# Optimization experiments

Hardware: AMD Instinct MI355X
Metric: run time of the kernel (lower is better)

## Reference

```python
import jax, jax.numpy as jnp
import numpy as np

B, D, H, L, P, IMG = 8, 768, 12, 12, 16, 448
GRID = 28  # pos_embed grid (785 = 1 + 28*28)
EPS = 1e-5


def layer_norm(x, g, b):
    mu = jnp.mean(x, axis=-1, keepdims=True)
    var = jnp.mean((x - mu) ** 2, axis=-1, keepdims=True)
    return (x - mu) * jax.lax.rsqrt(var + EPS) * g + b


def setup_inputs() -> dict:
    key = jax.random.key(0)
    ks = jax.random.split(key, 12)
    s = 0.02
    inp = {
        "x": jax.random.normal(ks[0], (B, 3, IMG, IMG), dtype=jnp.float32),
        "conv_w": jax.random.normal(ks[1], (D, 3, P, P), dtype=jnp.float32) * s,
        "conv_b": jnp.zeros((D,), jnp.float32),
        "cls_token": jax.random.normal(ks[2], (1, 1, D), dtype=jnp.float32) * s,
        "pos_embed": jax.random.normal(ks[3], (1, 1 + GRID * GRID, D), dtype=jnp.float32) * s,
        "ln1_g": jnp.ones((L, D), jnp.float32),
        "ln1_b": jnp.zeros((L, D), jnp.float32),
        "qkv_w": jax.random.normal(ks[4], (L, D, 3 * D), dtype=jnp.float32) * s,
        "qkv_b": jnp.zeros((L, 3 * D), jnp.float32),
        "proj_w": jax.random.normal(ks[5], (L, D, D), dtype=jnp.float32) * s,
        "proj_b": jnp.zeros((L, D), jnp.float32),
        "ln2_g": jnp.ones((L, D), jnp.float32),
        "ln2_b": jnp.zeros((L, D), jnp.float32),
        "mlp_w1": jax.random.normal(ks[6], (L, D, 4 * D), dtype=jnp.float32) * s,
        "mlp_b1": jnp.zeros((L, 4 * D), jnp.float32),
        "mlp_w2": jax.random.normal(ks[7], (L, 4 * D, D), dtype=jnp.float32) * s,
        "mlp_b2": jnp.zeros((L, D), jnp.float32),
        "lnf_g": jnp.ones((D,), jnp.float32),
        "lnf_b": jnp.zeros((D,), jnp.float32),
    }
    return inp


def _vit_forward(x, conv_w, conv_b, cls_token, pos_embed,
                 ln1_g, ln1_b, qkv_w, qkv_b, proj_w, proj_b,
                 ln2_g, ln2_b, mlp_w1, mlp_b1, mlp_w2, mlp_b2, lnf_g, lnf_b):
    b = x.shape[0]
    # PatchEmbed: strided conv -> [B, D, 28, 28] -> [B, N, D]
    h = jax.lax.conv_general_dilated(
        x, conv_w, window_strides=(P, P), padding="VALID",
        dimension_numbers=("NCHW", "OIHW", "NCHW")) + conv_b[None, :, None, None]
    gh, gw = h.shape[2], h.shape[3]
    h = h.reshape(b, D, gh * gw).transpose(0, 2, 1)  # [B, N, D]
    # ClassEmbed
    h = jnp.concatenate([jnp.broadcast_to(cls_token, (b, 1, D)), h], axis=1)
    # PosEmbed with bicubic interpolation of the grid part (identity when gh=gw=28)
    grid = pos_embed[:, 1:, :].transpose(0, 2, 1).reshape(1, D, GRID, GRID)
    grid = jax.image.resize(grid, (1, D, gh, gw), method="bicubic")
    grid = grid.reshape(1, D, gh * gw).transpose(0, 2, 1)
    pos = jnp.concatenate([pos_embed[:, :1, :], grid], axis=1)
    h = h + pos

    scale = (D // H) ** (-0.5)

    def block(h, p):
        (l1g, l1b, qw, qb, pw, pb, l2g, l2b, w1, b1, w2, b2) = p
        y = layer_norm(h, l1g, l1b)
        m, n, d = y.shape
        qkv = (y @ qw + qb).reshape(m, n, 3, H, d // H)
        qkv = qkv.transpose(2, 0, 3, 1, 4)  # [3, B, H, N, dh]
        q, k, v = qkv[0], qkv[1], qkv[2]
        w = jax.nn.softmax(jnp.einsum("bhnd,bhmd->bhnm", q, k) * scale, axis=-1)
        attn = jnp.einsum("bhnm,bhmd->bhnd", w, v).transpose(0, 2, 1, 3).reshape(m, n, d)
        h = h + (attn @ pw + pb)
        y = layer_norm(h, l2g, l2b)
        h = h + (jax.nn.gelu(y @ w1 + b1, approximate=False) @ w2 + b2)
        return h, None

    params = (ln1_g, ln1_b, qkv_w, qkv_b, proj_w, proj_b,
              ln2_g, ln2_b, mlp_w1, mlp_b1, mlp_w2, mlp_b2)
    h, _ = jax.lax.scan(block, h, params)
    return layer_norm(h, lnf_g, lnf_b)[:, 0]


def reference(x, conv_w, conv_b, cls_token, pos_embed,
              ln1_g, ln1_b, qkv_w, qkv_b, proj_w, proj_b,
              ln2_g, ln2_b, mlp_w1, mlp_b1, mlp_w2, mlp_b2, lnf_g, lnf_b):
    return _vit_forward(x, conv_w, conv_b, cls_token, pos_embed,
                        ln1_g, ln1_b, qkv_w, qkv_b, proj_w, proj_b,
                        ln2_g, ln2_b, mlp_w1, mlp_b1, mlp_w2, mlp_b2, lnf_g, lnf_b)
```

## Files before the change

kernel.cpp:

```cpp
#include <hip/hip_runtime.h>
#include <math.h>

#define B_   8
#define D_   768
#define H_   12
#define L_   12
#define NTOK 785
#define NPAT 784
#define MTOT (B_ * NTOK)
#define MPAT (B_ * NPAT)
#define MPAD 6400
#define DFF  3072
#define EPS_ 1e-5f

typedef unsigned short u16;
typedef unsigned int   u32;
typedef short s16x8 __attribute__((ext_vector_type(8)));
typedef float f32x4 __attribute__((ext_vector_type(4)));

__device__ __forceinline__ u16 f2b(float f) {
    u32 u = __float_as_uint(f);
    u += 0x7fffu + ((u >> 16) & 1u);
    return (u16)(u >> 16);
}
__device__ __forceinline__ float b2f(u16 s) {
    return __uint_as_float(((u32)s) << 16);
}
__device__ __forceinline__ void gload_lds16(const void* g, void* l) {
    __builtin_amdgcn_global_load_lds(
        (const __attribute__((address_space(1))) void*)g,
        (__attribute__((address_space(3))) void*)l, 16, 0, 0);
}
__device__ __forceinline__ float gelu_exact(float x) {
    return 0.5f * x * (1.0f + erff(x * 0.70710678118654752f));
}

template <int BM, int MODE, int OUTBF>
__global__ __launch_bounds__(256) void mfma_gemm(
    const u16* __restrict__ A, const u16* __restrict__ WT,
    const float* __restrict__ bias, const float* __restrict__ R,
    void* __restrict__ Cout, int M, int N, int K)
{
    constexpr int MI = BM / 32;
    __shared__ u16 As[2][BM * 32];
    __shared__ u16 Bs[2][128 * 32];

    const int bm = blockIdx.y * BM;
    const int bn = blockIdx.x * 128;
    const int t  = threadIdx.x;
    const int wv = t >> 6, ln = t & 63;
    const int wr = wv >> 1, wc = wv & 1;

    f32x4 acc[MI][4];
    const f32x4 z4 = {0.f, 0.f, 0.f, 0.f};
#pragma unroll
    for (int i = 0; i < MI; i++)
#pragma unroll
        for (int j = 0; j < 4; j++) acc[i][j] = z4;

    const int lrow = ln & 15;
    const int sq   = ((ln >> 4) ^ (ln & 3)) * 8;
    const int ssl  = ((ln & 3) ^ ((ln >> 2) & 3)) * 8;

    auto stage = [&](int kt, int buf) {
#pragma unroll
        for (int g = 0; g < BM / 64; g++) {
            const int c = g * 256 + wv * 64 + ln;
            const int r = c >> 2;
            u16* ldsA = As[buf] + (g * 256 + wv * 64) * 8;
            gload_lds16(A + (size_t)(bm + r) * K + kt + ssl, ldsA);
        }
#pragma unroll
        for (int g = 0; g < 2; g++) {
            const int c = g * 256 + wv * 64 + ln;
            const int r = c >> 2;
            u16* ldsB = Bs[buf] + (g * 256 + wv * 64) * 8;
            gload_lds16(WT + (size_t)(bn + r) * K + kt + ssl, ldsB);
        }
    };

    stage(0, 0);
    __syncthreads();
    int cur = 0;

    for (int kt = 0; kt < K; kt += 32) {
        if (kt + 32 < K) stage(kt + 32, cur ^ 1);

        s16x8 af[MI], bf[4];
#pragma unroll
        for (int i = 0; i < MI; i++)
            af[i] = *(const s16x8*)(As[cur] + (wr * (BM / 2) + i * 16 + lrow) * 32 + sq);
#pragma unroll
        for (int j = 0; j < 4; j++)
            bf[j] = *(const s16x8*)(Bs[cur] + (wc * 64 + j * 16 + lrow) * 32 + sq);
#pragma unroll
        for (int i = 0; i < MI; i++)
#pragma unroll
            for (int j = 0; j < 4; j++)
                acc[i][j] = __builtin_amdgcn_mfma_f32_16x16x32_bf16(
                    af[i], bf[j], acc[i][j], 0, 0, 0);

        __syncthreads();
        cur ^= 1;
    }

    const int col_l = ln & 15;
    const int rq    = (ln >> 4) * 4;
#pragma unroll
    for (int j = 0; j < 4; j++) {
        const int col = bn + wc * 64 + j * 16 + col_l;
        const float bj = bias[col];
#pragma unroll
        for (int i = 0; i < MI; i++) {
            const int row0 = bm + wr * (BM / 2) + i * 16 + rq;
#pragma unroll
            for (int rg = 0; rg < 4; rg++) {
                const int row = row0 + rg;
                if (row >= M) continue;
                float v = acc[i][j][rg] + bj;
                if (MODE == 1) v = gelu_exact(v);
                if (MODE == 2) v += R[(size_t)row * N + col];
                if (OUTBF) ((u16*)Cout)[(size_t)row * N + col] = f2b(v);
                else       ((float*)Cout)[(size_t)row * N + col] = v;
            }
        }
    }
}

__global__ __launch_bounds__(256) void wt_kernel(
    const float* __restrict__ W, u16* __restrict__ WT, int K, int N)
{
    const size_t lz = blockIdx.z;
    W  += lz * (size_t)K * N;
    WT += lz * (size_t)K * N;
    __shared__ float tile[32][33];
    const int n0 = blockIdx.x * 32, k0 = blockIdx.y * 32;
    const int r = threadIdx.x >> 3, c4 = (threadIdx.x & 7) * 4;
    const float4 v = *(const float4*)(W + (size_t)(k0 + r) * N + n0 + c4);
    tile[r][c4 + 0] = v.x; tile[r][c4 + 1] = v.y;
    tile[r][c4 + 2] = v.z; tile[r][c4 + 3] = v.w;
    __syncthreads();
    ushort4 o = make_ushort4(f2b(tile[c4 + 0][r]), f2b(tile[c4 + 1][r]),
                             f2b(tile[c4 + 2][r]), f2b(tile[c4 + 3][r]));
    *(ushort4*)(WT + (size_t)(n0 + r) * K + k0 + c4) = o;
}

__global__ __launch_bounds__(256) void flatcvt_kernel(
    const float* __restrict__ in, u16* __restrict__ out, int n4)
{
    const int i = blockIdx.x * 256 + threadIdx.x;
    if (i >= n4) return;
    const float4 v = ((const float4*)in)[i];
    ((ushort4*)out)[i] = make_ushort4(f2b(v.x), f2b(v.y), f2b(v.z), f2b(v.w));
}

__device__ __forceinline__ float block_sum(float s, float* red) {
#pragma unroll
    for (int off = 32; off; off >>= 1) s += __shfl_down(s, off, 64);
    const int wid = threadIdx.x >> 6;
    if ((threadIdx.x & 63) == 0) red[wid] = s;
    __syncthreads();
    if (threadIdx.x == 0) red[0] = red[0] + red[1] + red[2] + red[3];
    __syncthreads();
    const float r = red[0];
    __syncthreads();
    return r;
}

template <int OUTBF>
__global__ __launch_bounds__(256) void ln_kernel(
    const float* __restrict__ X, const float* __restrict__ g,
    const float* __restrict__ b, void* __restrict__ Y, size_t row_stride_in)
{
    __shared__ float red[4];
    const int row = blockIdx.x;
    const int t = threadIdx.x;
    const float* x = X + (size_t)row * row_stride_in;

    const float v0 = x[t], v1 = x[t + 256], v2 = x[t + 512];
    const float mean = block_sum(v0 + v1 + v2, red) * (1.0f / 768.0f);
    const float d0 = v0 - mean, d1 = v1 - mean, d2 = v2 - mean;
    const float var = block_sum(d0 * d0 + d1 * d1 + d2 * d2, red) * (1.0f / 768.0f);
    const float rs = rsqrtf(var + EPS_);

    const float o0 = d0 * rs * g[t] + b[t];
    const float o1 = d1 * rs * g[t + 256] + b[t + 256];
    const float o2 = d2 * rs * g[t + 512] + b[t + 512];
    if (OUTBF) {
        u16* y = (u16*)Y + (size_t)row * 768;
        y[t] = f2b(o0); y[t + 256] = f2b(o1); y[t + 512] = f2b(o2);
    } else {
        float* y = (float*)Y + (size_t)row * 768;
        y[t] = o0; y[t + 256] = o1; y[t + 512] = o2;
    }
}

#define AQB  128
#define AKT  64
#define KSTR 72

__global__ __launch_bounds__(256) void attn_kernel(
    const u16* __restrict__ qkv, u16* __restrict__ out)
{
    __shared__ u16 Ks[AKT * KSTR];
    __shared__ u16 Vt[64 * KSTR];
    __shared__ u16 Ps[4 * 32 * KSTR];

    const int bh = blockIdx.y;
    const int b  = bh / H_, hh = bh % H_;
    const int q0 = blockIdx.x * AQB;
    const int t  = threadIdx.x;
    const int w  = t >> 6, ln = t & 63;
    const int lrow = ln & 15, quad = ln >> 4;
    const size_t tokbase = (size_t)b * NTOK;

    s16x8 aq[2][2];
#pragma unroll
    for (int rowt = 0; rowt < 2; rowt++) {
        int qr = q0 + w * 32 + rowt * 16 + lrow;
        if (qr > NTOK - 1) qr = NTOK - 1;
        const u16* qp = qkv + (tokbase + qr) * 2304 + hh * 64 + quad * 8;
        aq[rowt][0] = *(const s16x8*)(qp);
        aq[rowt][1] = *(const s16x8*)(qp + 32);
    }

    f32x4 acc_o[2][4];
    const f32x4 z4 = {0.f, 0.f, 0.f, 0.f};
#pragma unroll
    for (int i = 0; i < 2; i++)
#pragma unroll
        for (int j = 0; j < 4; j++) acc_o[i][j] = z4;
    float m_r[2][4], l_r[2][4];
#pragma unroll
    for (int i = 0; i < 2; i++)
#pragma unroll
        for (int j = 0; j < 4; j++) { m_r[i][j] = -1e30f; l_r[i][j] = 0.f; }

    for (int j0 = 0; j0 < NTOK; j0 += AKT) {
        __syncthreads();
#pragma unroll
        for (int g = 0; g < 2; g++) {
            const int c = g * 256 + t;
            const int j = c >> 3, dc = c & 7;
            int jj = j0 + j; if (jj > NTOK - 1) jj = NTOK - 1;
            const s16x8 kv = *(const s16x8*)(
                qkv + (tokbase + jj) * 2304 + 768 + hh * 64 + dc * 8);
            *(s16x8*)(Ks + j * KSTR + dc * 8) = kv;
        }
#pragma unroll
        for (int g = 0; g < 2; g++) {
            const int c = g * 256 + t;
            const int j = c & 63, dc = c >> 6;
            int jj = j0 + j; if (jj > NTOK - 1) jj = NTOK - 1;
            const s16x8 vv = *(const s16x8*)(
                qkv + (tokbase + jj) * 2304 + 1536 + hh * 64 + dc * 8);
#pragma unroll
            for (int e = 0; e < 8; e++)
                Vt[(dc * 8 + e) * KSTR + j] = (u16)((const short*)&vv)[e];
        }
        __syncthreads();

        f32x4 acc_s[2][4];
#pragma unroll
        for (int i = 0; i < 2; i++)
#pragma unroll
            for (int j = 0; j < 4; j++) acc_s[i][j] = z4;
#pragma unroll
        for (int jt = 0; jt < 4; jt++) {
            const s16x8 bk0 =
                *(const s16x8*)(Ks + (jt * 16 + lrow) * KSTR + quad * 8);
            const s16x8 bk1 =
                *(const s16x8*)(Ks + (jt * 16 + lrow) * KSTR + 32 + quad * 8);
#pragma unroll
            for (int rowt = 0; rowt < 2; rowt++) {
                acc_s[rowt][jt] = __builtin_amdgcn_mfma_f32_16x16x32_bf16(
                    aq[rowt][0], bk0, acc_s[rowt][jt], 0, 0, 0);
                acc_s[rowt][jt] = __builtin_amdgcn_mfma_f32_16x16x32_bf16(
                    aq[rowt][1], bk1, acc_s[rowt][jt], 0, 0, 0);
            }
        }
        const f32x4 ninf = {-1e30f, -1e30f, -1e30f, -1e30f};
#pragma unroll
        for (int jt = 0; jt < 4; jt++) {
            const bool valid = (j0 + jt * 16 + lrow) < NTOK;
#pragma unroll
            for (int rowt = 0; rowt < 2; rowt++)
                acc_s[rowt][jt] = valid ? acc_s[rowt][jt] * 0.125f : ninf;
        }

#pragma unroll
        for (int rowt = 0; rowt < 2; rowt++) {
#pragma unroll
            for (int rg = 0; rg < 4; rg++) {
                float mx = fmaxf(fmaxf(acc_s[rowt][0][rg], acc_s[rowt][1][rg]),
                                 fmaxf(acc_s[rowt][2][rg], acc_s[rowt][3][rg]));
                mx = fmaxf(mx, __shfl_xor(mx, 1, 64));
                mx = fmaxf(mx, __shfl_xor(mx, 2, 64));
                mx = fmaxf(mx, __shfl_xor(mx, 4, 64));
                mx = fmaxf(mx, __shfl_xor(mx, 8, 64));
                const float nm = fmaxf(m_r[rowt][rg], mx);
                const float al = __expf(m_r[rowt][rg] - nm);
                m_r[rowt][rg] = nm;
                u16* prow = Ps + (size_t)(w * 32 + rowt * 16 + quad * 4 + rg) * KSTR
                            + lrow;
                float ps = 0.f;
#pragma unroll
                for (int jt = 0; jt < 4; jt++) {
                    const float p = __expf(acc_s[rowt][jt][rg] - nm);
                    ps += p;
                    prow[jt * 16] = f2b(p);
                }
                ps += __shfl_xor(ps, 1, 64);
                ps += __shfl_xor(ps, 2, 64);
                ps += __shfl_xor(ps, 4, 64);
                ps += __shfl_xor(ps, 8, 64);
                l_r[rowt][rg] = l_r[rowt][rg] * al + ps;
#pragma unroll
                for (int dt = 0; dt < 4; dt++) acc_o[rowt][dt][rg] *= al;
            }
        }

#pragma unroll
        for (int jc = 0; jc < 2; jc++) {
            const s16x8 ap0 = *(const s16x8*)(
                Ps + (w * 32 + lrow) * KSTR + jc * 32 + quad * 8);
            const s16x8 ap1 = *(const s16x8*)(
                Ps + (w * 32 + 16 + lrow) * KSTR + jc * 32 + quad * 8);
#pragma unroll
            for (int dt = 0; dt < 4; dt++) {
                const s16x8 bv = *(const s16x8*)(
                    Vt + (dt * 16 + lrow) * KSTR + jc * 32 + quad * 8);
                acc_o[0][dt] = __builtin_amdgcn_mfma_f32_16x16x32_bf16(
                    ap0, bv, acc_o[0][dt], 0, 0, 0);
                acc_o[1][dt] = __builtin_amdgcn_mfma_f32_16x16x32_bf16(
                    ap1, bv, acc_o[1][dt], 0, 0, 0);
            }
        }
    }

#pragma unroll
    for (int rowt = 0; rowt < 2; rowt++) {
#pragma unroll
        for (int rg = 0; rg < 4; rg++) {
            const int tok = q0 + w * 32 + rowt * 16 + quad * 4 + rg;
            if (tok >= NTOK) continue;
            const float inv = 1.0f / l_r[rowt][rg];
            u16* dst = out + (tokbase + tok) * D_ + hh * 64 + lrow;
#pragma unroll
            for (int dt = 0; dt < 4; dt++)
                dst[dt * 16] = f2b(acc_o[rowt][dt][rg] * inv);
        }
    }
}

__global__ __launch_bounds__(256) void im2col_kernel(
    const float* __restrict__ x, u16* __restrict__ patches)
{
    const int idx = blockIdx.x * 256 + threadIdx.x;
    if (idx >= MPAT * 96) return;
    const int prow = idx / 96;
    const int c8 = (idx % 96) * 8;
    const int bb = prow / NPAT;
    const int pp = prow % NPAT;
    const int gy = pp / 28, gx = pp % 28;
    const int c = c8 >> 8;
    const int rem = c8 & 255;
    const int py = rem >> 4, px = rem & 15;
    const float* src =
        x + (((size_t)(bb * 3 + c) * 448 + gy * 16 + py) * 448 + gx * 16 + px);
    const float4 a = *(const float4*)src;
    const float4 bq = *(const float4*)(src + 4);
    u16* dst = patches + (size_t)prow * 768 + c8;
    uint4 w4;
    w4.x = (u32)f2b(a.x) | ((u32)f2b(a.y) << 16);
    w4.y = (u32)f2b(a.z) | ((u32)f2b(a.w) << 16);
    w4.z = (u32)f2b(bq.x) | ((u32)f2b(bq.y) << 16);
    w4.w = (u32)f2b(bq.z) | ((u32)f2b(bq.w) << 16);
    *(uint4*)dst = w4;
}

__global__ __launch_bounds__(256) void assemble_kernel(
    const float* __restrict__ conv_out, const float* __restrict__ cls,
    const float* __restrict__ pos, float* __restrict__ h)
{
    const int idx = blockIdx.x * 256 + threadIdx.x;
    if (idx >= MTOT * 192) return;
    const int row = idx / 192;
    const int d = (idx % 192) * 4;
    const int bb = row / NTOK, n = row % NTOK;
    const float4 pv = *(const float4*)(pos + (size_t)n * 768 + d);
    float4 v;
    if (n == 0) {
        const float4 cv = *(const float4*)(cls + d);
        v = make_float4(cv.x + pv.x, cv.y + pv.y, cv.z + pv.z, cv.w + pv.w);
    } else {
        const float4 co =
            *(const float4*)(conv_out + (size_t)(bb * NPAT + n - 1) * 768 + d);
        v = make_float4(co.x + pv.x, co.y + pv.y, co.z + pv.z, co.w + pv.w);
    }
    *(float4*)(h + (size_t)row * 768 + d) = v;
}

extern "C" void kernel_launch(void* const* d_in, const int* in_sizes, int n_in,
                              void* d_out, int out_size, void* d_ws, size_t ws_size,
                              hipStream_t stream)
{
    const float* x      = (const float*)d_in[0];
    const float* conv_w = (const float*)d_in[1];
    const float* conv_b = (const float*)d_in[2];
    const float* cls    = (const float*)d_in[3];
    const float* pos    = (const float*)d_in[4];
    const float* ln1_g  = (const float*)d_in[5];
    const float* ln1_b  = (const float*)d_in[6];
    const float* qkv_w  = (const float*)d_in[7];
    const float* qkv_b  = (const float*)d_in[8];
    const float* proj_w = (const float*)d_in[9];
    const float* proj_b = (const float*)d_in[10];
    const float* ln2_g  = (const float*)d_in[11];
    const float* ln2_b  = (const float*)d_in[12];
    const float* w1     = (const float*)d_in[13];
    const float* b1     = (const float*)d_in[14];
    const float* w2     = (const float*)d_in[15];
    const float* b2     = (const float*)d_in[16];
    const float* lnf_g  = (const float*)d_in[17];
    const float* lnf_b  = (const float*)d_in[18];
    float* out = (float*)d_out;

    auto al = [](size_t v) { return (v + 255) & ~(size_t)255; };

    const size_t base_need =
        al((size_t)MPAD * 768 * 4) + al((size_t)MPAD * 768 * 2) +
        al((size_t)MPAD * 2304 * 2) + al((size_t)MPAD * 768 * 2) +
        al((size_t)MPAD * 3072 * 2) + al((size_t)768 * 768 * 2) + 4096;
    const size_t per_layer_w =
        al((size_t)2304 * 768 * 2) + al((size_t)768 * 768 * 2) +
        al((size_t)3072 * 768 * 2) + al((size_t)768 * 3072 * 2);
    const bool batched = ws_size >= base_need + 12 * per_layer_w;
    const int LW = batched ? 12 : 1;

    char* p = (char*)d_ws;
    auto alloc = [&](size_t bytes) {
        char* r = p;
        p += (bytes + 255) & ~(size_t)255;
        return r;
    };
    float* h    = (float*)alloc((size_t)MPAD * 768 * 4);
    u16*  y     = (u16*)alloc((size_t)MPAD * 768 * 2);
    u16*  qkv   = (u16*)alloc((size_t)MPAD * 2304 * 2);
    u16*  attn  = (u16*)alloc((size_t)MPAD * 768 * 2);
    u16*  mid   = (u16*)alloc((size_t)MPAD * 3072 * 2);
    u16*  wq    = (u16*)alloc((size_t)LW * 2304 * 768 * 2);
    u16*  wp    = (u16*)alloc((size_t)LW * 768 * 768 * 2);
    u16*  w1t   = (u16*)alloc((size_t)LW * 3072 * 768 * 2);
    u16*  w2t   = (u16*)alloc((size_t)LW * 768 * 3072 * 2);
    u16*  wcv   = (u16*)alloc((size_t)768 * 768 * 2);
    (void)alloc(4096);
    u16*   patches = mid;
    float* cbuf    = (float*)qkv;

    const dim3 blk(256);

    flatcvt_kernel<<<(768 * 768 / 4 + 255) / 256, blk, 0, stream>>>(conv_w, wcv,
                                                                    768 * 768 / 4);
    im2col_kernel<<<(MPAT * 96 + 255) / 256, blk, 0, stream>>>(x, patches);
    mfma_gemm<64, 0, 0><<<dim3(6, MPAT / 64), blk, 0, stream>>>(
        patches, wcv, conv_b, nullptr, cbuf, MPAT, 768, 768);
    assemble_kernel<<<(MTOT * 192 + 255) / 256, blk, 0, stream>>>(cbuf, cls, pos, h);

    if (batched) {
        wt_kernel<<<dim3(2304 / 32, 768 / 32, 12), blk, 0, stream>>>(
            qkv_w, wq, 768, 2304);
        wt_kernel<<<dim3(768 / 32, 768 / 32, 12), blk, 0, stream>>>(
            proj_w, wp, 768, 768);
        wt_kernel<<<dim3(3072 / 32, 768 / 32, 12), blk, 0, stream>>>(
            w1, w1t, 768, 3072);
        wt_kernel<<<dim3(768 / 32, 3072 / 32, 12), blk, 0, stream>>>(
            w2, w2t, 3072, 768);
    }

    const int my64 = (MTOT + 63) / 64;

    for (int l = 0; l < L_; l++) {
        u16* wq_l  = wq  + (size_t)(batched ? l : 0) * 2304 * 768;
        u16* wp_l  = wp  + (size_t)(batched ? l : 0) * 768 * 768;
        u16* w1t_l = w1t + (size_t)(batched ? l : 0) * 3072 * 768;
        u16* w2t_l = w2t + (size_t)(batched ? l : 0) * 768 * 3072;
        if (!batched) {
            wt_kernel<<<dim3(2304 / 32, 768 / 32), blk, 0, stream>>>(
                qkv_w + (size_t)l * 768 * 2304, wq_l, 768, 2304);
            wt_kernel<<<dim3(768 / 32, 768 / 32), blk, 0, stream>>>(
                proj_w + (size_t)l * 768 * 768, wp_l, 768, 768);
            wt_kernel<<<dim3(3072 / 32, 768 / 32), blk, 0, stream>>>(
                w1 + (size_t)l * 768 * 3072, w1t_l, 768, 3072);
            wt_kernel<<<dim3(768 / 32, 3072 / 32), blk, 0, stream>>>(
                w2 + (size_t)l * 3072 * 768, w2t_l, 3072, 768);
        }

        ln_kernel<1><<<MTOT, blk, 0, stream>>>(h, ln1_g + l * 768, ln1_b + l * 768,
                                               y, 768);
        mfma_gemm<128, 0, 1><<<dim3(18, 50), blk, 0, stream>>>(
            y, wq_l, qkv_b + l * 2304, nullptr, qkv, MTOT, 2304, 768);
        attn_kernel<<<dim3((NTOK + AQB - 1) / AQB, B_ * H_), blk, 0, stream>>>(
            qkv, attn);
        mfma_gemm<64, 2, 0><<<dim3(6, my64), blk, 0, stream>>>(
            attn, wp_l, proj_b + l * 768, h, h, MTOT, 768, 768);
        ln_kernel<1><<<MTOT, blk, 0, stream>>>(h, ln2_g + l * 768, ln2_b + l * 768,
                                               y, 768);
        mfma_gemm<128, 1, 1><<<dim3(24, 50), blk, 0, stream>>>(
            y, w1t_l, b1 + l * DFF, nullptr, mid, MTOT, DFF, 768);
        mfma_gemm<64, 2, 0><<<dim3(6, my64), blk, 0, stream>>>(
            mid, w2t_l, b2 + l * 768, h, h, MTOT, 768, DFF);
    }

    ln_kernel<0><<<B_, blk, 0, stream>>>(h, lnf_g, lnf_b, out, (size_t)NTOK * 768);
}
```

Baseline: 4.331 ms.

## Triple-buffer GEMM LDS staging with partial vmcnt waits

Moves the MFMA GEMM from double to triple buffering in LDS, so loads run two k-steps ahead. Each step waits only for the oldest batch of global-to-LDS loads via a partial vmcnt and a raw barrier, instead of a full __syncthreads drain. This is meant to hide global load latency behind MFMA work. It costs more LDS per block, which may reduce occupancy, and relies on hand-encoded waitcnt values being correct for this target.

```diff
diff --git a/kernel.cpp b/kernel.cpp
--- a/kernel.cpp
+++ b/kernel.cpp
@@ -35,15 +35,28 @@
     return 0.5f * x * (1.0f + erff(x * 0.70710678118654752f));
 }
 
+template <int N>
+__device__ __forceinline__ void wait_vm() {
+    if constexpr (N == 0)      __builtin_amdgcn_s_waitcnt(0x0F70);
+    else if constexpr (N == 3) __builtin_amdgcn_s_waitcnt(0x0F73);
+    else if constexpr (N == 4) __builtin_amdgcn_s_waitcnt(0x0F74);
+    __builtin_amdgcn_sched_barrier(0);
+}
+__device__ __forceinline__ void bar_raw() {
+    __builtin_amdgcn_s_barrier();
+    __builtin_amdgcn_sched_barrier(0);
+}
+
 template <int BM, int MODE, int OUTBF>
 __global__ __launch_bounds__(256) void mfma_gemm(
     const u16* __restrict__ A, const u16* __restrict__ WT,
     const float* __restrict__ bias, const float* __restrict__ R,
     void* __restrict__ Cout, int M, int N, int K)
 {
-    constexpr int MI = BM / 32;
-    __shared__ u16 As[2][BM * 32];
-    __shared__ u16 Bs[2][128 * 32];
+    constexpr int MI  = BM / 32;
+    constexpr int LPB = BM / 64 + 2;
+    __shared__ u16 As[3][BM * 32];
+    __shared__ u16 Bs[3][128 * 32];
 
     const int bm = blockIdx.y * BM;
     const int bn = blockIdx.x * 128;
@@ -79,30 +92,42 @@
         }
     };
 
-    stage(0, 0);
-    __syncthreads();
-    int cur = 0;
-
-    for (int kt = 0; kt < K; kt += 32) {
-        if (kt + 32 < K) stage(kt + 32, cur ^ 1);
-
+    auto compute = [&](int buf) {
         s16x8 af[MI], bf[4];
 #pragma unroll
         for (int i = 0; i < MI; i++)
-            af[i] = *(const s16x8*)(As[cur] + (wr * (BM / 2) + i * 16 + lrow) * 32 + sq);
+            af[i] = *(const s16x8*)(As[buf] + (wr * (BM / 2) + i * 16 + lrow) * 32 + sq);
 #pragma unroll
         for (int j = 0; j < 4; j++)
-            bf[j] = *(const s16x8*)(Bs[cur] + (wc * 64 + j * 16 + lrow) * 32 + sq);
+            bf[j] = *(const s16x8*)(Bs[buf] + (wc * 64 + j * 16 + lrow) * 32 + sq);
 #pragma unroll
         for (int i = 0; i < MI; i++)
 #pragma unroll
             for (int j = 0; j < 4; j++)
                 acc[i][j] = __builtin_amdgcn_mfma_f32_16x16x32_bf16(
                     af[i], bf[j], acc[i][j], 0, 0, 0);
-
-        __syncthreads();
-        cur ^= 1;
-    }
+    };
+
+    stage(0, 0);
+    stage(32, 1);
+    wait_vm<LPB>();
+    bar_raw();
+
+    int cur = 0;
+    int kt  = 0;
+    for (; kt + 64 < K; kt += 32) {
+        int nb = cur + 2; if (nb >= 3) nb -= 3;
+        stage(kt + 64, nb);
+        compute(cur);
+        wait_vm<LPB>();
+        bar_raw();
+        cur = cur + 1; if (cur >= 3) cur -= 3;
+    }
+    compute(cur);
+    wait_vm<0>();
+    bar_raw();
+    cur = cur + 1; if (cur >= 3) cur -= 3;
+    compute(cur);
 
     const int col_l = ln & 15;
     const int rq    = (ln >> 4) * 4;
```

Measured after the change: 4.416 ms. Within noise of the previous version (+2.0%).
